# Kernel optimization log

Measured on AMD Instinct MI355X. Metric: run time of the kernel, lower is better.

The kernel has to match this reference:

```python
import jax, jax.numpy as jnp
import numpy as np

D_MODEL = 1024
NHEAD = 16
DK = D_MODEL // NHEAD  # 64
B, S = 2, 2048


def setup_inputs() -> dict:
    key = jax.random.key(0)
    ks = jax.random.split(key, 8)
    Q = jax.random.normal(ks[0], (B, S, D_MODEL), dtype=jnp.float32)
    K = jax.random.normal(ks[1], (B, S, D_MODEL), dtype=jnp.float32)
    V = jax.random.normal(ks[2], (B, S, D_MODEL), dtype=jnp.float32)
    additive_mask = jax.random.normal(ks[3], (S, S), dtype=jnp.float32)
    key_padding_mask = jnp.zeros((B, S), dtype=jnp.int32)  # ignored by the module
    # Per-head projection weights, stacked over heads: [H, d_model, dk]
    scale = 1.0 / np.sqrt(D_MODEL)
    WQ = jax.random.normal(ks[4], (NHEAD, D_MODEL, DK), dtype=jnp.float32) * scale
    WK = jax.random.normal(ks[5], (NHEAD, D_MODEL, DK), dtype=jnp.float32) * scale
    WV = jax.random.normal(ks[6], (NHEAD, D_MODEL, DK), dtype=jnp.float32) * scale
    WO = jax.random.normal(ks[7], (D_MODEL, D_MODEL), dtype=jnp.float32) * scale
    return {"Q": Q, "K": K, "V": V, "additive_mask": additive_mask,
            "key_padding_mask": key_padding_mask,
            "WQ": WQ, "WK": WK, "WV": WV, "WO": WO}


def reference(Q, K, V, additive_mask, key_padding_mask, WQ, WK, WV, WO):
    # Per-head projections, batched over heads: [B, H, S, dk]
    q = jnp.einsum('bsd,hdk->bhsk', Q, WQ)
    k = jnp.einsum('bsd,hdk->bhsk', K, WK)
    v = jnp.einsum('bsd,hdk->bhsk', V, WV)
    # scores: [B, H, S, S]; mask broadcasts over batch and head
    scores = jnp.einsum('bhqk,bhsk->bhqs', q, k) / np.sqrt(DK)
    scores = scores + additive_mask[None, None, :, :]
    attn = jax.nn.softmax(scores, axis=-1)
    o = jnp.einsum('bhqs,bhsk->bhqk', attn, v)  # [B, H, S, dk]
    # concat heads in head order == transpose + reshape to [B, S, H*dk]
    o = o.transpose(0, 2, 1, 3).reshape(Q.shape[0], Q.shape[1], D_MODEL)
    return o @ WO
```

## Files before the change

kernel.cpp:

```cpp
#include <hip/hip_runtime.h>
#include <hip/hip_bf16.h>
#include <stdint.h>

#define D_MODEL 1024
#define NHEAD 16
#define DKH 64
#define BATCH 2
#define SEQ 2048
#define LOG2E 1.44269504088896f

typedef __bf16 bf16_t;
typedef __bf16 bf16x8 __attribute__((ext_vector_type(8)));
typedef float f32x4 __attribute__((ext_vector_type(4)));
typedef float f32x16 __attribute__((ext_vector_type(16)));

__device__ __forceinline__ float fast_exp2(float x) {
#if __has_builtin(__builtin_amdgcn_exp2f)
  return __builtin_amdgcn_exp2f(x);
#else
  return exp2f(x);
#endif
}

__device__ __forceinline__ void gload_lds16(const bf16_t* g, bf16_t* l) {
  auto gp = (const __attribute__((address_space(1))) void*)(uintptr_t)g;
  auto lp = (__attribute__((address_space(3))) void*)(uintptr_t)l;
  __builtin_amdgcn_global_load_lds(gp, lp, 16, 0, 0);
}

__device__ __forceinline__ uint32_t pkbf(float lo, float hi) {
  bf16_t a = (bf16_t)lo, c = (bf16_t)hi;
  uint16_t ua, uc;
  __builtin_memcpy(&ua, &a, 2);
  __builtin_memcpy(&uc, &c, 2);
  return (uint32_t)ua | ((uint32_t)uc << 16);
}

__device__ __forceinline__ void perm32swap(uint32_t& a, uint32_t& b) {
  asm volatile("v_permlane32_swap_b32 %0, %1" : "+v"(a), "+v"(b));
}

__global__ void k_cvt3(const float* __restrict__ Q, const float* __restrict__ K,
                       const float* __restrict__ V, bf16_t* __restrict__ out) {
  const float* in = blockIdx.y == 0 ? Q : (blockIdx.y == 1 ? K : V);
  int i = (blockIdx.x * 256 + threadIdx.x) * 8;
  float4 a = *reinterpret_cast<const float4*>(in + i);
  float4 b = *reinterpret_cast<const float4*>(in + i + 4);
  bf16x8 o;
  o[0] = (bf16_t)a.x; o[1] = (bf16_t)a.y; o[2] = (bf16_t)a.z; o[3] = (bf16_t)a.w;
  o[4] = (bf16_t)b.x; o[5] = (bf16_t)b.y; o[6] = (bf16_t)b.z; o[7] = (bf16_t)b.w;
  *reinterpret_cast<bf16x8*>(out + (size_t)blockIdx.y * BATCH * SEQ * D_MODEL + i) = o;
}

__global__ void k_cvtw(const float* __restrict__ WQ, const float* __restrict__ WK,
                       const float* __restrict__ WV, const float* __restrict__ WO,
                       bf16_t* __restrict__ wt) {
  int j = blockIdx.x * 256 + threadIdx.x;
  int d = j & 1023, n = j >> 10;
  if (n < 3072) {
    int proj = n >> 10, h = (n >> 6) & 15, k = n & 63;
    const float* w = proj == 0 ? WQ : (proj == 1 ? WK : WV);
    float scale = proj == 0 ? (0.125f * LOG2E) : 1.0f;
    wt[j] = (bf16_t)(w[(h << 16) + (d << 6) + k] * scale);
  } else {
    wt[j] = (bf16_t)WO[(d << 10) + (n - 3072)];
  }
}

__global__ void k_maskg(const float* __restrict__ M, bf16_t* __restrict__ Mf) {
  int t = blockIdx.x * 256 + threadIdx.x;
  int wch = t & 7, lane = (t >> 3) & 63;
  int kvt = (t >> 9) & 31, qt = t >> 14;
  int h = lane >> 5, ql = lane & 31;
  int q = qt * 32 + ql;
  int t32 = wch >> 2, r2 = wch & 3;
  int kvb = kvt * 64 + t32 * 32 + 8 * r2 + 4 * h;
  float4 m4 = *reinterpret_cast<const float4*>(M + (size_t)q * SEQ + kvb);
  bf16_t o[4];
  o[0] = (bf16_t)(m4.x * LOG2E); o[1] = (bf16_t)(m4.y * LOG2E);
  o[2] = (bf16_t)(m4.z * LOG2E); o[3] = (bf16_t)(m4.w * LOG2E);
  *reinterpret_cast<ushort4*>(Mf + (size_t)t * 4) = *reinterpret_cast<ushort4*>(o);
}

__global__ __launch_bounds__(256)
void k_gemm_qkv(const bf16_t* __restrict__ A, const bf16_t* __restrict__ Bt,
                bf16_t* __restrict__ qh, bf16_t* __restrict__ Kf,
                bf16_t* __restrict__ Vf) {
  __shared__ __align__(16) bf16_t As[128 * 32];
  __shared__ __align__(16) bf16_t Bs[128 * 32];
  const int tid = threadIdx.x;
  const int lane = tid & 63, wave = tid >> 6;
  const int g = lane >> 4, lr = lane & 15;
  const int bm = blockIdx.x, bn = blockIdx.y;
  const int pn = bn >> 3;
  const bf16_t* Ap = A + (size_t)pn * (BATCH * SEQ * D_MODEL);
  const int wm = (wave >> 1) << 6, wn = (wave & 1) << 6;
  f32x4 acc[4][4] = {};

  for (int kt = 0; kt < 1024; kt += 32) {
#pragma unroll
    for (int cc = 0; cc < 2; cc++) {
      int c = tid + cc * 256;
      int row = c >> 2, ko = (c & 3) << 3;
      gload_lds16(Ap + (size_t)(bm * 128 + row) * 1024 + kt + ko, As + c * 8);
      gload_lds16(Bt + (size_t)(bn * 128 + row) * 1024 + kt + ko, Bs + c * 8);
    }
    __syncthreads();
    bf16x8 af[4], bfr[4];
#pragma unroll
    for (int t = 0; t < 4; t++)
      af[t] = *reinterpret_cast<const bf16x8*>(As + (wm + t * 16 + lr) * 32 + g * 8);
#pragma unroll
    for (int t = 0; t < 4; t++)
      bfr[t] = *reinterpret_cast<const bf16x8*>(Bs + (wn + t * 16 + lr) * 32 + g * 8);
    __builtin_amdgcn_s_setprio(1);
#pragma unroll
    for (int i = 0; i < 4; i++)
#pragma unroll
      for (int j = 0; j < 4; j++)
        acc[i][j] = __builtin_amdgcn_mfma_f32_16x16x32_bf16(af[i], bfr[j], acc[i][j], 0, 0, 0);
    __builtin_amdgcn_s_setprio(0);
    __syncthreads();
  }

#pragma unroll
  for (int i = 0; i < 4; i++)
#pragma unroll
    for (int j = 0; j < 4; j++)
#pragma unroll
      for (int e = 0; e < 4; e++) {
        int row = (bm << 7) + wm + i * 16 + g * 4 + e;
        int col = ((bn & 7) << 7) + wn + j * 16 + lr;
        float v = acc[i][j][e];
        int b = row >> 11, s = row & 2047, h = col >> 6, d = col & 63;
        size_t bh32 = (size_t)((b << 4) + h) * 32;
        if (pn == 0) {
          qh[((size_t)(((b << 4) + h) * SEQ + s) << 6) + d] = (bf16_t)v;
        } else if (pn == 1) {
          int kt2 = s >> 6, u = s & 63, t32 = u >> 5, ql2 = u & 31;
          int kk2 = d >> 4, hq2 = (d >> 3) & 1, e2 = d & 7;
          Kf[(bh32 + kt2) * 4096 + (t32 * 4 + kk2) * 512 + (hq2 * 32 + ql2) * 8 + e2] = (bf16_t)v;
        } else {
          int kt2 = s >> 6, u = s & 63, s2 = u >> 4, hq2 = (u >> 3) & 1, e2 = u & 7;
          int dkt = d >> 5, ql2 = d & 31;
          Vf[(bh32 + kt2) * 4096 + (dkt * 4 + s2) * 512 + (hq2 * 32 + ql2) * 8 + e2] = (bf16_t)v;
        }
      }
}

__global__ __launch_bounds__(256)
void k_gemm_wo(const bf16_t* __restrict__ A, const bf16_t* __restrict__ Bt,
               float* __restrict__ C) {
  __shared__ __align__(16) bf16_t As[64 * 32];
  __shared__ __align__(16) bf16_t Bs[128 * 32];
  const int tid = threadIdx.x;
  const int lane = tid & 63, wave = tid >> 6;
  const int g = lane >> 4, lr = lane & 15;
  const int bm = blockIdx.x, bn = blockIdx.y;
  const int wm = (wave >> 1) << 5, wn = (wave & 1) << 6;
  f32x4 acc[2][4] = {};

  for (int kt = 0; kt < 1024; kt += 32) {
    {
      int row = tid >> 2, ko = (tid & 3) << 3;
      gload_lds16(A + (size_t)(bm * 64 + row) * 1024 + kt + ko, As + tid * 8);
    }
#pragma unroll
    for (int cc = 0; cc < 2; cc++) {
      int c = tid + cc * 256;
      int row = c >> 2, ko = (c & 3) << 3;
      gload_lds16(Bt + (size_t)(bn * 128 + row) * 1024 + kt + ko, Bs + c * 8);
    }
    __syncthreads();
    bf16x8 af[2], bfr[4];
#pragma unroll
    for (int t = 0; t < 2; t++)
      af[t] = *reinterpret_cast<const bf16x8*>(As + (wm + t * 16 + lr) * 32 + g * 8);
#pragma unroll
    for (int t = 0; t < 4; t++)
      bfr[t] = *reinterpret_cast<const bf16x8*>(Bs + (wn + t * 16 + lr) * 32 + g * 8);
    __builtin_amdgcn_s_setprio(1);
#pragma unroll
    for (int i = 0; i < 2; i++)
#pragma unroll
      for (int j = 0; j < 4; j++)
        acc[i][j] = __builtin_amdgcn_mfma_f32_16x16x32_bf16(af[i], bfr[j], acc[i][j], 0, 0, 0);
    __builtin_amdgcn_s_setprio(0);
    __syncthreads();
  }
#pragma unroll
  for (int i = 0; i < 2; i++)
#pragma unroll
    for (int j = 0; j < 4; j++)
#pragma unroll
      for (int e = 0; e < 4; e++) {
        int row = (bm << 6) + wm + i * 16 + g * 4 + e;
        int col = (bn << 7) + wn + j * 16 + lr;
        C[(size_t)row * D_MODEL + col] = acc[i][j][e];
      }
}

__global__ __launch_bounds__(512, 4)
void k_attn6(const bf16_t* __restrict__ Qh, const bf16_t* __restrict__ Kf,
             const bf16_t* __restrict__ Vf, const bf16_t* __restrict__ Mf,
             bf16_t* __restrict__ O) {
  __shared__ __align__(16) bf16_t Ks[2][2][4096];
  __shared__ __align__(16) bf16_t Vs[2][2][4096];
  const int bh = blockIdx.y, b = bh >> 4, h = bh & 15;
  const int tid = threadIdx.x, w = tid >> 6, lane = tid & 63;
  const int qw = w & 3, hh = w >> 2;
  const int hq = lane >> 5, ql = lane & 31;
  const int tid256 = tid & 255;
  const int qbase = blockIdx.x * 128 + qw * 32;
  const bf16_t* qp = Qh + (size_t)bh * SEQ * DKH;
  const bf16_t* kfp = Kf + (size_t)bh * 32 * 4096;
  const bf16_t* vfp = Vf + (size_t)bh * 32 * 4096;
  const int qt = blockIdx.x * 4 + qw;
  const bf16_t* mp = Mf + ((size_t)(qt * 32 + hh * 16) * 64 + lane) * 32;
  const int NIT = 16;

  bf16x8 aq[4];
#pragma unroll
  for (int kk = 0; kk < 4; kk++)
    aq[kk] = *reinterpret_cast<const bf16x8*>(
        qp + (size_t)(qbase + ql) * DKH + kk * 16 + hq * 8);

  f32x16 oacc[2] = {};
  float lsum = 0.f;

  auto stage = [&](int buf, int kt) {
#pragma unroll
    for (int cc = 0; cc < 2; cc++) {
      int c = tid256 + cc * 256;
      gload_lds16(kfp + (size_t)kt * 4096 + c * 8, &Ks[hh][buf][c * 8]);
      gload_lds16(vfp + (size_t)kt * 4096 + c * 8, &Vs[hh][buf][c * 8]);
    }
  };

  stage(0, hh * 16);
  bf16x8 mv[4];
#pragma unroll
  for (int j = 0; j < 4; j++)
    mv[j] = *reinterpret_cast<const bf16x8*>(mp + j * 8);
  __syncthreads();

  for (int it = 0; it < NIT; ++it) {
    const int cur = it & 1;
    if (it + 1 < NIT) stage(cur ^ 1, hh * 16 + it + 1);

    const bf16_t* kb = Ks[hh][cur];
    const bf16_t* vb = Vs[hh][cur];

    f32x16 p[2];
#pragma unroll
    for (int t32 = 0; t32 < 2; t32++) {
      f32x16 a = {};
      __builtin_amdgcn_s_setprio(1);
#pragma unroll
      for (int kk = 0; kk < 4; kk++) {
        bf16x8 bk = *reinterpret_cast<const bf16x8*>(kb + (t32 * 4 + kk) * 512 + lane * 8);
        a = __builtin_amdgcn_mfma_f32_32x32x16_bf16(bk, aq[kk], a, 0, 0, 0);
      }
      __builtin_amdgcn_s_setprio(0);
      p[t32] = a;
    }

    bf16x8 paf[4];
#pragma unroll
    for (int s = 0; s < 4; s++) {
      const int t32 = s >> 1, rb = (s & 1) * 8;
      float pes[8];
#pragma unroll
      for (int j = 0; j < 8; j++) {
        int v = t32 * 16 + rb + j;
        float x = p[t32][rb + j] + (float)mv[v >> 3][v & 7];
        float pe = fast_exp2(x);
        lsum += pe;
        pes[j] = pe;
      }
      uint32_t u0 = pkbf(pes[0], pes[1]), u1 = pkbf(pes[2], pes[3]);
      uint32_t w0 = pkbf(pes[4], pes[5]), w1 = pkbf(pes[6], pes[7]);
      perm32swap(u0, w0);
      perm32swap(u1, w1);
      union { uint32_t wd[4]; bf16x8 v8; } fu;
      fu.wd[0] = u0; fu.wd[1] = u1; fu.wd[2] = w0; fu.wd[3] = w1;
      paf[s] = fu.v8;
    }

    {
      const bf16_t* mn = mp + (size_t)((it + 1 < NIT) ? (it + 1) : it) * 2048;
#pragma unroll
      for (int j = 0; j < 4; j++)
        mv[j] = *reinterpret_cast<const bf16x8*>(mn + j * 8);
    }

#pragma unroll
    for (int dkt = 0; dkt < 2; dkt++) {
      __builtin_amdgcn_s_setprio(1);
#pragma unroll
      for (int s = 0; s < 4; s++) {
        bf16x8 bv = *reinterpret_cast<const bf16x8*>(vb + (dkt * 4 + s) * 512 + lane * 8);
        oacc[dkt] = __builtin_amdgcn_mfma_f32_32x32x16_bf16(paf[s], bv, oacc[dkt], 0, 0, 0);
      }
      __builtin_amdgcn_s_setprio(0);
    }
    __syncthreads();
  }

  float* smO = (float*)&Ks[0][0][0];
  float* smL = (float*)&Vs[0][0][0];
  if (w >= 4) {
    int base = (qw * 64 + lane) * 32;
#pragma unroll
    for (int dkt = 0; dkt < 2; dkt++)
#pragma unroll
      for (int cg = 0; cg < 4; cg++) {
        int chs = ((dkt * 4 + cg) ^ (lane & 7)) * 4;
        float4 val = {oacc[dkt][cg * 4], oacc[dkt][cg * 4 + 1],
                      oacc[dkt][cg * 4 + 2], oacc[dkt][cg * 4 + 3]};
        *reinterpret_cast<float4*>(&smO[base + chs]) = val;
      }
    smL[qw * 64 + lane] = lsum;
  }
  __syncthreads();
  if (w < 4) {
    int base = (qw * 64 + lane) * 32;
#pragma unroll
    for (int dkt = 0; dkt < 2; dkt++)
#pragma unroll
      for (int cg = 0; cg < 4; cg++) {
        int chs = ((dkt * 4 + cg) ^ (lane & 7)) * 4;
        float4 pv = *reinterpret_cast<const float4*>(&smO[base + chs]);
#pragma unroll
        for (int e = 0; e < 4; e++) oacc[dkt][cg * 4 + e] += pv[e];
      }
    lsum += smL[qw * 64 + lane];
    float lf = lsum + __shfl_xor(lsum, 32);
    float inv[16];
#pragma unroll
    for (int reg = 0; reg < 16; reg++) {
      int qrow = (reg & 3) + 8 * (reg >> 2) + 4 * hq;
      inv[reg] = 1.0f / __shfl(lf, qrow);
    }
#pragma unroll
    for (int dkt = 0; dkt < 2; dkt++)
#pragma unroll
      for (int reg = 0; reg < 16; reg++) {
        int qrow = (reg & 3) + 8 * (reg >> 2) + 4 * hq;
        float v = oacc[dkt][reg] * inv[reg];
        O[(size_t)(b * SEQ + qbase + qrow) * D_MODEL + (h << 6) + dkt * 32 + ql] = (bf16_t)v;
      }
  }
}

extern "C" void kernel_launch(void* const* d_in, const int* in_sizes, int n_in,
                              void* d_out, int out_size, void* d_ws, size_t ws_size,
                              hipStream_t stream) {
  const float* Q  = (const float*)d_in[0];
  const float* K  = (const float*)d_in[1];
  const float* V  = (const float*)d_in[2];
  const float* M  = (const float*)d_in[3];
  const float* WQ = (const float*)d_in[5];
  const float* WK = (const float*)d_in[6];
  const float* WV = (const float*)d_in[7];
  const float* WO = (const float*)d_in[8];

  char* ws = (char*)d_ws;
  const size_t MB = 1 << 20;
  bf16_t* Qb    = (bf16_t*)(ws + 0 * MB);
  bf16_t* Mf    = (bf16_t*)(ws + 24 * MB);
  bf16_t* WqkvT = (bf16_t*)(ws + 32 * MB);
  bf16_t* WoT   = (bf16_t*)(ws + 38 * MB);
  bf16_t* qh    = (bf16_t*)(ws + 40 * MB);
  bf16_t* Kf    = (bf16_t*)(ws + 48 * MB);
  bf16_t* Vf    = (bf16_t*)(ws + 56 * MB);
  bf16_t* Ob    = (bf16_t*)(ws + 64 * MB);

  k_cvt3<<<dim3(2048, 3), 256, 0, stream>>>(Q, K, V, Qb);
  k_maskg<<<4096, 256, 0, stream>>>(M, Mf);
  k_cvtw<<<16384, 256, 0, stream>>>(WQ, WK, WV, WO, WqkvT);

  k_gemm_qkv<<<dim3(32, 24), 256, 0, stream>>>(Qb, WqkvT, qh, Kf, Vf);

  k_attn6<<<dim3(16, 32), 512, 0, stream>>>(qh, Kf, Vf, Mf, Ob);

  k_gemm_wo<<<dim3(64, 8), 256, 0, stream>>>(Ob, WoT, (float*)d_out);
}
```

Baseline: 156.8 us.

## Fuse fp32-to-bf16 input conversion into QKV GEMM; compute row sums via MFMA

Drops the separate k_cvt3 pass and has the QKV GEMM load fp32 activations directly into registers, convert them to bf16 and write them to LDS, with a one-step register prefetch of the next K tile. This removes a full kernel launch plus the write and reread of a bf16 copy of Q/K/V. The cost is that each A tile is now re-read in fp32 by every one of the 8 column blocks of its projection, doubling the A-side global traffic. Separately, the attention kernel now computes softmax row sums with an extra MFMA against a vector of ones instead of scalar adds and shuffles, trading VALU and shuffle work for additional MFMA issue and LDS traffic in the final reduction.

```diff
diff --git a/kernel.cpp b/kernel.cpp
--- a/kernel.cpp
+++ b/kernel.cpp
@@ -38,18 +38,6 @@
 
 __device__ __forceinline__ void perm32swap(uint32_t& a, uint32_t& b) {
   asm volatile("v_permlane32_swap_b32 %0, %1" : "+v"(a), "+v"(b));
-}
-
-__global__ void k_cvt3(const float* __restrict__ Q, const float* __restrict__ K,
-                       const float* __restrict__ V, bf16_t* __restrict__ out) {
-  const float* in = blockIdx.y == 0 ? Q : (blockIdx.y == 1 ? K : V);
-  int i = (blockIdx.x * 256 + threadIdx.x) * 8;
-  float4 a = *reinterpret_cast<const float4*>(in + i);
-  float4 b = *reinterpret_cast<const float4*>(in + i + 4);
-  bf16x8 o;
-  o[0] = (bf16_t)a.x; o[1] = (bf16_t)a.y; o[2] = (bf16_t)a.z; o[3] = (bf16_t)a.w;
-  o[4] = (bf16_t)b.x; o[5] = (bf16_t)b.y; o[6] = (bf16_t)b.z; o[7] = (bf16_t)b.w;
-  *reinterpret_cast<bf16x8*>(out + (size_t)blockIdx.y * BATCH * SEQ * D_MODEL + i) = o;
 }
 
 __global__ void k_cvtw(const float* __restrict__ WQ, const float* __restrict__ WK,
@@ -83,7 +71,8 @@
 }
 
 __global__ __launch_bounds__(256)
-void k_gemm_qkv(const bf16_t* __restrict__ A, const bf16_t* __restrict__ Bt,
+void k_gemm_qkv(const float* __restrict__ Qs, const float* __restrict__ Ks32,
+                const float* __restrict__ Vs32, const bf16_t* __restrict__ Bt,
                 bf16_t* __restrict__ qh, bf16_t* __restrict__ Kf,
                 bf16_t* __restrict__ Vf) {
   __shared__ __align__(16) bf16_t As[128 * 32];
@@ -93,17 +82,39 @@
   const int g = lane >> 4, lr = lane & 15;
   const int bm = blockIdx.x, bn = blockIdx.y;
   const int pn = bn >> 3;
-  const bf16_t* Ap = A + (size_t)pn * (BATCH * SEQ * D_MODEL);
+  const float* Ap32 = pn == 0 ? Qs : (pn == 1 ? Ks32 : Vs32);
   const int wm = (wave >> 1) << 6, wn = (wave & 1) << 6;
+  const int arow = tid >> 1, ako = (tid & 1) << 4;
+  const float* aptr = Ap32 + (size_t)(bm * 128 + arow) * 1024 + ako;
   f32x4 acc[4][4] = {};
+
+  float4 fA0 = *reinterpret_cast<const float4*>(aptr);
+  float4 fA1 = *reinterpret_cast<const float4*>(aptr + 4);
+  float4 fA2 = *reinterpret_cast<const float4*>(aptr + 8);
+  float4 fA3 = *reinterpret_cast<const float4*>(aptr + 12);
 
   for (int kt = 0; kt < 1024; kt += 32) {
 #pragma unroll
     for (int cc = 0; cc < 2; cc++) {
       int c = tid + cc * 256;
       int row = c >> 2, ko = (c & 3) << 3;
-      gload_lds16(Ap + (size_t)(bm * 128 + row) * 1024 + kt + ko, As + c * 8);
       gload_lds16(Bt + (size_t)(bn * 128 + row) * 1024 + kt + ko, Bs + c * 8);
+    }
+    {
+      bf16x8 o0, o1;
+      o0[0] = (bf16_t)fA0.x; o0[1] = (bf16_t)fA0.y; o0[2] = (bf16_t)fA0.z; o0[3] = (bf16_t)fA0.w;
+      o0[4] = (bf16_t)fA1.x; o0[5] = (bf16_t)fA1.y; o0[6] = (bf16_t)fA1.z; o0[7] = (bf16_t)fA1.w;
+      o1[0] = (bf16_t)fA2.x; o1[1] = (bf16_t)fA2.y; o1[2] = (bf16_t)fA2.z; o1[3] = (bf16_t)fA2.w;
+      o1[4] = (bf16_t)fA3.x; o1[5] = (bf16_t)fA3.y; o1[6] = (bf16_t)fA3.z; o1[7] = (bf16_t)fA3.w;
+      *reinterpret_cast<bf16x8*>(As + arow * 32 + ako) = o0;
+      *reinterpret_cast<bf16x8*>(As + arow * 32 + ako + 8) = o1;
+    }
+    if (kt + 32 < 1024) {
+      const float* np = aptr + kt + 32;
+      fA0 = *reinterpret_cast<const float4*>(np);
+      fA1 = *reinterpret_cast<const float4*>(np + 4);
+      fA2 = *reinterpret_cast<const float4*>(np + 8);
+      fA3 = *reinterpret_cast<const float4*>(np + 12);
     }
     __syncthreads();
     bf16x8 af[4], bfr[4];
@@ -226,7 +237,9 @@
         qp + (size_t)(qbase + ql) * DKH + kk * 16 + hq * 8);
 
   f32x16 oacc[2] = {};
-  float lsum = 0.f;
+  f32x16 lacc = {};
+  const bf16_t onev = (bf16_t)1.0f;
+  const bf16x8 ones = {onev, onev, onev, onev, onev, onev, onev, onev};
 
   auto stage = [&](int buf, int kt) {
 #pragma unroll
@@ -274,9 +287,7 @@
       for (int j = 0; j < 8; j++) {
         int v = t32 * 16 + rb + j;
         float x = p[t32][rb + j] + (float)mv[v >> 3][v & 7];
-        float pe = fast_exp2(x);
-        lsum += pe;
-        pes[j] = pe;
+        pes[j] = fast_exp2(x);
       }
       uint32_t u0 = pkbf(pes[0], pes[1]), u1 = pkbf(pes[2], pes[3]);
       uint32_t w0 = pkbf(pes[4], pes[5]), w1 = pkbf(pes[6], pes[7]);
@@ -285,6 +296,7 @@
       union { uint32_t wd[4]; bf16x8 v8; } fu;
       fu.wd[0] = u0; fu.wd[1] = u1; fu.wd[2] = w0; fu.wd[3] = w1;
       paf[s] = fu.v8;
+      lacc = __builtin_amdgcn_mfma_f32_32x32x16_bf16(paf[s], ones, lacc, 0, 0, 0);
     }
 
     {
@@ -320,7 +332,13 @@
                       oacc[dkt][cg * 4 + 2], oacc[dkt][cg * 4 + 3]};
         *reinterpret_cast<float4*>(&smO[base + chs]) = val;
       }
-    smL[qw * 64 + lane] = lsum;
+    int lb = (qw * 64 + lane) * 16;
+#pragma unroll
+    for (int cg = 0; cg < 4; cg++) {
+      int chs = (cg ^ (lane & 3)) * 4;
+      float4 lv = {lacc[cg * 4], lacc[cg * 4 + 1], lacc[cg * 4 + 2], lacc[cg * 4 + 3]};
+      *reinterpret_cast<float4*>(&smL[lb + chs]) = lv;
+    }
   }
   __syncthreads();
   if (w < 4) {
@@ -334,14 +352,17 @@
 #pragma unroll
         for (int e = 0; e < 4; e++) oacc[dkt][cg * 4 + e] += pv[e];
       }
-    lsum += smL[qw * 64 + lane];
-    float lf = lsum + __shfl_xor(lsum, 32);
+    int lb = (qw * 64 + lane) * 16;
+#pragma unroll
+    for (int cg = 0; cg < 4; cg++) {
+      int chs = (cg ^ (lane & 3)) * 4;
+      float4 lv = *reinterpret_cast<const float4*>(&smL[lb + chs]);
+      lacc[cg * 4] += lv.x; lacc[cg * 4 + 1] += lv.y;
+      lacc[cg * 4 + 2] += lv.z; lacc[cg * 4 + 3] += lv.w;
+    }
     float inv[16];
 #pragma unroll
-    for (int reg = 0; reg < 16; reg++) {
-      int qrow = (reg & 3) + 8 * (reg >> 2) + 4 * hq;
-      inv[reg] = 1.0f / __shfl(lf, qrow);
-    }
+    for (int reg = 0; reg < 16; reg++) inv[reg] = 1.0f / lacc[reg];
 #pragma unroll
     for (int dkt = 0; dkt < 2; dkt++)
 #pragma unroll
@@ -367,7 +388,6 @@
 
   char* ws = (char*)d_ws;
   const size_t MB = 1 << 20;
-  bf16_t* Qb    = (bf16_t*)(ws + 0 * MB);
   bf16_t* Mf    = (bf16_t*)(ws + 24 * MB);
   bf16_t* WqkvT = (bf16_t*)(ws + 32 * MB);
   bf16_t* WoT   = (bf16_t*)(ws + 38 * MB);
@@ -376,11 +396,10 @@
   bf16_t* Vf    = (bf16_t*)(ws + 56 * MB);
   bf16_t* Ob    = (bf16_t*)(ws + 64 * MB);
 
-  k_cvt3<<<dim3(2048, 3), 256, 0, stream>>>(Q, K, V, Qb);
   k_maskg<<<4096, 256, 0, stream>>>(M, Mf);
   k_cvtw<<<16384, 256, 0, stream>>>(WQ, WK, WV, WO, WqkvT);
 
-  k_gemm_qkv<<<dim3(32, 24), 256, 0, stream>>>(Qb, WqkvT, qh, Kf, Vf);
+  k_gemm_qkv<<<dim3(32, 24), 256, 0, stream>>>(Q, K, V, WqkvT, qh, Kf, Vf);
 
   k_attn6<<<dim3(16, 32), 512, 0, stream>>>(qh, Kf, Vf, Mf, Ob);
 
```

Measured after the change: 159.4 us. Within noise of the previous version (+1.7%).
